# Performance work log

Measured on AMD Instinct MI355X. Metric: run time of the kernel, lower is better.

The kernel has to match this reference:

```python
import jax, jax.numpy as jnp
import numpy as np

B, L, H, X = 64, 512, 1024, 1024
D = H + X  # 2048


def setup_inputs() -> dict:
    key = jax.random.key(0)
    k = jax.random.split(key, 8)
    h_state = jax.random.normal(k[0], (B, L, H), dtype=jnp.float32)
    x = jax.random.normal(k[1], (B, L, X), dtype=jnp.float32)
    trigger = jax.random.randint(k[2], (B, 1), 0, L, dtype=jnp.int64)
    mask = jax.random.randint(k[3], (B, L), 0, 2, dtype=jnp.int32)
    # Linear params (torch Linear: y = x @ W.T + b)
    sa = 1.0 / np.sqrt(D)
    ss = 1.0 / np.sqrt(H)
    W_a = jax.random.uniform(k[4], (D, D), jnp.float32, -sa, sa)
    b_a = jax.random.uniform(k[5], (D,), jnp.float32, -sa, sa)
    W_s = jax.random.uniform(k[6], (D, H), jnp.float32, -ss, ss)
    b_s = jax.random.uniform(k[7], (D,), jnp.float32, -ss, ss)
    return {"h_state": h_state, "x": x, "W_a": W_a, "b_a": b_a,
            "W_s": W_s, "b_s": b_s, "trigger": trigger, "mask": mask}


def reference(h_state, x, W_a, b_a, W_s, b_s, trigger, mask):
    # a: [B, L, D]
    a = jnp.concatenate((h_state, x), axis=-1)
    # direct gather of the trigger position (replaces one_hot+masked_select)
    trig_a = jnp.take_along_axis(a, trigger[:, :, None], axis=1)  # [B, 1, D]
    s = h_state.sum(axis=1)  # [B, H]
    et = jnp.tanh(jnp.einsum('bld,ed->ble', a, W_a) + b_a
                  + (s @ W_s.T + b_s)[:, None, :])  # [B, L, D]
    et = jnp.where(mask[:, :, None] == 0, jnp.float32(-1e9), et)
    attn = jax.nn.softmax(et, axis=-1)  # softmax over feature dim D (as in source)
    # dropout is identity in eval mode
    out = (trig_a * attn).sum(axis=1)  # [B, D]
    return out
```

## Files before the change

kernel.cpp:

```cpp
#include <hip/hip_runtime.h>
#include <cstdint>

#define B_ 64
#define L_ 512
#define H_ 1024
#define D_ 2048

typedef __attribute__((ext_vector_type(8))) short short8;
typedef __attribute__((ext_vector_type(4))) float f32x4;
typedef unsigned int u32;

static __device__ __forceinline__ float bf2f(u32 lo16) {
    u32 u = lo16 << 16;
    return __builtin_bit_cast(float, u);
}
static __device__ __forceinline__ unsigned short f2bf(float f) {
    u32 u = __builtin_bit_cast(u32, f);
    u += 0x7fffu + ((u >> 16) & 1u);
    return (unsigned short)(u >> 16);
}
static __device__ __forceinline__ u32 pk(float x, float y) {
    return (u32)f2bf(x) | ((u32)f2bf(y) << 16);
}
static __device__ __forceinline__ float fast_pexp(float u) {
    u = fminf(15.f, fmaxf(-15.f, u));
    float ex = __expf(2.f * u);
    float th = (ex - 1.f) / (ex + 1.f);
    return __expf(th);
}
static __device__ __forceinline__ void gload_lds16(const unsigned short* g, unsigned short* l) {
    __builtin_amdgcn_global_load_lds((const __attribute__((address_space(1))) u32*)g,
                                     (__attribute__((address_space(3))) u32*)l, 16, 0, 0);
}

__global__ __launch_bounds__(256) void k_s(const float* __restrict__ h, float* __restrict__ s) {
    int t = blockIdx.x * 256 + threadIdx.x;
    int b = t >> 10, hh = t & 1023;
    const float* p = h + ((size_t)b * L_) * H_ + hh;
    float acc = 0.f;
#pragma unroll 8
    for (int l = 0; l < L_; ++l) acc += p[(size_t)l * H_];
    s[t] = acc;
}

__global__ __launch_bounds__(256) void k_compact(const int* __restrict__ mask,
                                                 const float* __restrict__ ba,
                                                 const float* __restrict__ bs,
                                                 int* __restrict__ ridx,
                                                 int* __restrict__ cnt1,
                                                 float* __restrict__ cnt0,
                                                 float* __restrict__ t2) {
    int b = blockIdx.x;
    __shared__ int sm[L_];
    for (int l = threadIdx.x; l < L_; l += 256) sm[l] = mask[b * L_ + l];
    for (int e = threadIdx.x; e < D_; e += 256) t2[b * D_ + e] = ba[e] + bs[e];
    __syncthreads();
    if (threadIdx.x == 0) {
        int* rb = ridx + b * L_;
        int c = 0;
        for (int l = 0; l < L_; ++l) if (sm[l]) rb[c++] = l;
        int n1 = c;
        int last = (c > 0) ? rb[c - 1] : 0;
        for (; c < L_; ++c) rb[c] = last;
        cnt1[b] = n1;
        cnt0[b] = (float)(L_ - n1);
    }
}

__global__ __launch_bounds__(256) void k_cvtW(const float* __restrict__ Wa,
                                              unsigned short* __restrict__ Wb) {
    int t = blockIdx.x * 256 + threadIdx.x;
    float4 v = ((const float4*)Wa)[t];
    ((uint2*)Wb)[t] = make_uint2(pk(v.x, v.y), pk(v.z, v.w));
}

__global__ __launch_bounds__(256) void k_prep(const float* __restrict__ hs, const float* __restrict__ xx,
                                              const int* __restrict__ ridx, const int* __restrict__ cnt1,
                                              unsigned short* __restrict__ Abf) {
    int j = blockIdx.x;
    int b = blockIdx.y;
    int n1 = cnt1[b];
    if (j >= ((n1 + 255) & ~255)) return;
    int l = ridx[b * L_ + j];
    int t = threadIdx.x;
    size_t rb = ((size_t)(b * L_ + l)) << 10;
    const float* src = (t < 128) ? (hs + rb + t * 8) : (xx + rb + (t - 128) * 8);
    float4 v0 = *(const float4*)src;
    float4 v1 = *(const float4*)(src + 4);
    *(uint4*)(Abf + (((size_t)(b * L_ + j)) << 11) + t * 8) =
        make_uint4(pk(v0.x, v0.y), pk(v0.z, v0.w), pk(v1.x, v1.y), pk(v1.z, v1.w));
}

__global__ __launch_bounds__(256) void k_t2(const float* __restrict__ s, const float* __restrict__ Ws,
                                            float* __restrict__ t2) {
    __shared__ float As[16][64];
    __shared__ float Bs[16][64];
    int n0 = blockIdx.x * 64;
    int ks0 = blockIdx.y * 256;
    int tid = threadIdx.x;
    int tx = tid & 15, ty = tid >> 4;
    int r = tid >> 2, q = tid & 3;
    float acc[4][4] = {};
    for (int k0 = ks0; k0 < ks0 + 256; k0 += 16) {
        float4 av = *(const float4*)(s + (size_t)r * H_ + k0 + q * 4);
        float4 bv = *(const float4*)(Ws + (size_t)(n0 + r) * H_ + k0 + q * 4);
        __syncthreads();
        As[q*4+0][r] = av.x; As[q*4+1][r] = av.y; As[q*4+2][r] = av.z; As[q*4+3][r] = av.w;
        Bs[q*4+0][r] = bv.x; Bs[q*4+1][r] = bv.y; Bs[q*4+2][r] = bv.z; Bs[q*4+3][r] = bv.w;
        __syncthreads();
#pragma unroll
        for (int kk = 0; kk < 16; ++kk) {
            float a_[4], b_[4];
            *(float4*)&a_[0] = *(const float4*)&As[kk][ty * 4];
            *(float4*)&b_[0] = *(const float4*)&Bs[kk][tx * 4];
#pragma unroll
            for (int i = 0; i < 4; ++i)
#pragma unroll
                for (int j = 0; j < 4; ++j) acc[i][j] += a_[i] * b_[j];
        }
    }
#pragma unroll
    for (int i = 0; i < 4; ++i)
#pragma unroll
        for (int j = 0; j < 4; ++j)
            atomicAdd(&t2[(size_t)(ty * 4 + i) * D_ + n0 + tx * 4 + j], acc[i][j]);
}

#define BAR3() do { asm volatile("" ::: "memory"); __builtin_amdgcn_s_barrier(); asm volatile("" ::: "memory"); } while (0)

__global__ __launch_bounds__(512, 2) void k_gemm3(
    const unsigned short* __restrict__ Abf, const unsigned short* __restrict__ Wb,
    const float* __restrict__ t2, const int* __restrict__ cnt1,
    float* __restrict__ rowsum, unsigned short* __restrict__ P)
{
    __shared__ unsigned short lds[65536];

    int tid = threadIdx.x;
    int lane = tid & 63;
    int w = tid >> 6;
    int wm = w >> 2;
    int wn = w & 3;
    int g = lane >> 4;
    int cl = lane & 15;

    int n0 = blockIdx.x * 256;
    int jt = blockIdx.y;
    int b = jt >> 1;
    int j0 = (jt & 1) * 256;
    int n1 = cnt1[b];
    if (j0 >= n1) return;

    int sr = w * 16 + (lane & 15);
    int sce = ((lane >> 4) & 3) * 8;
    const unsigned short* aS0 = Abf + (((size_t)(b * L_ + j0 + sr)) << 11) + sce;
    const unsigned short* aS1 = aS0 + ((size_t)128 << 11);
    const unsigned short* bS0 = Wb + (((size_t)(n0 + sr)) << 11) + sce;
    const unsigned short* bS1 = bS0 + ((size_t)128 << 11);
    int wq = w * 512;

#define STAGE_A3(h, tk, u) do { \
        const unsigned short* s_ = ((h) ? aS1 : aS0) + (tk) * 64; \
        unsigned short* d_ = &lds[(u) * 32768 + (h) * 8192 + wq]; \
        gload_lds16(s_, d_); gload_lds16(s_ + 32, d_ + 4096); } while (0)
#define STAGE_B3(h, tk, u) do { \
        const unsigned short* s_ = ((h) ? bS1 : bS0) + (tk) * 64; \
        unsigned short* d_ = &lds[(u) * 32768 + 16384 + (h) * 8192 + wq]; \
        gload_lds16(s_, d_); gload_lds16(s_ + 32, d_ + 4096); } while (0)

    int rdA = wm * 8192 + g * 128 + cl * 8;
    int rdB = 16384 + (wn >> 1) * 8192 + (wn & 1) * 2048 + g * 128 + cl * 8;

    f32x4 acc[8][4] = {};
    short8 af[4][2], bf0[2][2], bf1[2][2];

    STAGE_A3(0, 0, 0); STAGE_B3(0, 0, 0); STAGE_B3(1, 0, 0); STAGE_A3(1, 0, 0);
    STAGE_B3(0, 1, 1); STAGE_B3(1, 1, 1); STAGE_A3(0, 1, 1);
    asm volatile("s_waitcnt vmcnt(6)" ::: "memory");
    BAR3();

    for (int t = 0; t < 32; ++t) {
        int u = t & 1;
        int ub = u * 32768;
        int tn = (t + 1) & 31, tnn = (t + 2) & 31;

#pragma unroll
        for (int m = 0; m < 4; ++m) {
            af[m][0] = *(const short8*)&lds[ub + rdA + m * 512];
            af[m][1] = *(const short8*)&lds[ub + rdA + 4096 + m * 512];
        }
#pragma unroll
        for (int n = 0; n < 2; ++n) {
            bf0[n][0] = *(const short8*)&lds[ub + rdB + n * 512];
            bf0[n][1] = *(const short8*)&lds[ub + rdB + 4096 + n * 512];
        }
        STAGE_A3(1, tn, u ^ 1);
        BAR3();
        __builtin_amdgcn_s_setprio(1);
#pragma unroll
        for (int m = 0; m < 4; ++m)
#pragma unroll
            for (int n = 0; n < 2; ++n) {
                acc[m][n] = __builtin_amdgcn_mfma_f32_16x16x32_bf16(af[m][0], bf0[n][0], acc[m][n], 0, 0, 0);
                acc[m][n] = __builtin_amdgcn_mfma_f32_16x16x32_bf16(af[m][1], bf0[n][1], acc[m][n], 0, 0, 0);
            }
        __builtin_amdgcn_s_setprio(0);
        BAR3();

#pragma unroll
        for (int n = 0; n < 2; ++n) {
            bf1[n][0] = *(const short8*)&lds[ub + rdB + (n + 2) * 512];
            bf1[n][1] = *(const short8*)&lds[ub + rdB + 4096 + (n + 2) * 512];
        }
        BAR3();
        __builtin_amdgcn_s_setprio(1);
#pragma unroll
        for (int m = 0; m < 4; ++m)
#pragma unroll
            for (int n = 0; n < 2; ++n) {
                acc[m][n + 2] = __builtin_amdgcn_mfma_f32_16x16x32_bf16(af[m][0], bf1[n][0], acc[m][n + 2], 0, 0, 0);
                acc[m][n + 2] = __builtin_amdgcn_mfma_f32_16x16x32_bf16(af[m][1], bf1[n][1], acc[m][n + 2], 0, 0, 0);
            }
        __builtin_amdgcn_s_setprio(0);
        BAR3();

#pragma unroll
        for (int m = 0; m < 4; ++m) {
            af[m][0] = *(const short8*)&lds[ub + rdA + (m + 4) * 512];
            af[m][1] = *(const short8*)&lds[ub + rdA + 4096 + (m + 4) * 512];
        }
        STAGE_B3(0, tnn, u);
        BAR3();
        __builtin_amdgcn_s_setprio(1);
#pragma unroll
        for (int m = 0; m < 4; ++m)
#pragma unroll
            for (int n = 0; n < 2; ++n) {
                acc[m + 4][n + 2] = __builtin_amdgcn_mfma_f32_16x16x32_bf16(af[m][0], bf1[n][0], acc[m + 4][n + 2], 0, 0, 0);
                acc[m + 4][n + 2] = __builtin_amdgcn_mfma_f32_16x16x32_bf16(af[m][1], bf1[n][1], acc[m + 4][n + 2], 0, 0, 0);
            }
        __builtin_amdgcn_s_setprio(0);
        BAR3();

        STAGE_B3(1, tnn, u);
        STAGE_A3(0, tnn, u);
        asm volatile("s_waitcnt vmcnt(6)" ::: "memory");
        BAR3();
        __builtin_amdgcn_s_setprio(1);
#pragma unroll
        for (int m = 0; m < 4; ++m)
#pragma unroll
            for (int n = 0; n < 2; ++n) {
                acc[m + 4][n] = __builtin_amdgcn_mfma_f32_16x16x32_bf16(af[m][0], bf0[n][0], acc[m + 4][n], 0, 0, 0);
                acc[m + 4][n] = __builtin_amdgcn_mfma_f32_16x16x32_bf16(af[m][1], bf0[n][1], acc[m + 4][n], 0, 0, 0);
            }
        __builtin_amdgcn_s_setprio(0);
        BAR3();
    }
#undef STAGE_A3
#undef STAGE_B3

    asm volatile("s_waitcnt vmcnt(0)" ::: "memory");
    __syncthreads();

    float t2v[4]; int ecol[4];
#pragma unroll
    for (int n = 0; n < 4; ++n) { ecol[n] = n0 + wn * 64 + n * 16 + cl; t2v[n] = t2[b * D_ + ecol[n]]; }
    int orow0 = b * L_ + j0 + wm * 128;
    int qd = g;

    float rs[8][4] = {};
#pragma unroll
    for (int m = 0; m < 8; ++m) {
        int lrowb = m * 16 + qd * 4;
#pragma unroll
        for (int n = 0; n < 4; ++n) {
#pragma unroll
            for (int gg = 0; gg < 4; ++gg) {
                float p = fast_pexp(acc[m][n][gg] + t2v[n]);
                rs[m][gg] += p;
                P[(size_t)(orow0 + lrowb + gg) * D_ + ecol[n]] = f2bf(p);
            }
        }
    }
#pragma unroll
    for (int m = 0; m < 8; ++m)
#pragma unroll
        for (int gg = 0; gg < 4; ++gg) {
            float v = rs[m][gg];
            v += __shfl_xor(v, 1); v += __shfl_xor(v, 2);
            v += __shfl_xor(v, 4); v += __shfl_xor(v, 8);
            rs[m][gg] = v;
        }
    float* red = (float*)lds;
    if (tid < 256) red[tid] = 0.f;
    __syncthreads();
    if (cl == 0) {
#pragma unroll
        for (int m = 0; m < 8; ++m)
#pragma unroll
            for (int gg = 0; gg < 4; ++gg)
                atomicAdd(&red[wm * 128 + m * 16 + qd * 4 + gg], rs[m][gg]);
    }
    __syncthreads();
    if (tid < 256) atomicAdd(&rowsum[b * L_ + j0 + tid], red[tid]);
}

__global__ __launch_bounds__(256) void k_fin2(const unsigned short* __restrict__ P,
                                              const float* __restrict__ rowsum,
                                              const int* __restrict__ cnt1,
                                              const int* __restrict__ trigger,
                                              const float* __restrict__ hs,
                                              const float* __restrict__ xx,
                                              float* __restrict__ out) {
    int b = blockIdx.y;
    __shared__ float iv[L_];
    int n1 = cnt1[b];
    int lceil = (n1 + 127) & ~127;
    for (int j = threadIdx.x; j < L_; j += 256)
        iv[j] = (j < n1) ? 1.f / rowsum[b * L_ + j] : 0.f;
    __syncthreads();
    int e0 = blockIdx.x * 512 + threadIdx.x * 2;
    const unsigned short* Pb = P + (((size_t)b) << 20) + e0;
    float s0 = 0.f, s1 = 0.f;
#pragma unroll 8
    for (int l = 0; l < lceil; ++l) {
        float f = iv[l];
        u32 pv = *(const u32*)(Pb + (((size_t)l) << 11));
        s0 += f * bf2f(pv & 0xffffu);
        s1 += f * bf2f(pv >> 16);
    }
    float base = (float)(L_ - n1) * (1.f / 2048.f);
    int trig = trigger[b];
    size_t tb = ((size_t)(b * L_ + trig)) << 10;
    float ta0 = (e0 < 1024) ? hs[tb + e0] : xx[tb + e0 - 1024];
    float ta1 = (e0 + 1 < 1024) ? hs[tb + e0 + 1] : xx[tb + e0 + 1 - 1024];
    out[b * D_ + e0]     = (s0 + base) * ta0;
    out[b * D_ + e0 + 1] = (s1 + base) * ta1;
}

#define BM 128
#define BN 128
#define BK 32
#define LDK 40
__global__ __launch_bounds__(256) void k_gemm(
    const float* __restrict__ hs, const float* __restrict__ xx,
    const float* __restrict__ Wa, const unsigned short* __restrict__ Wb,
    const float* __restrict__ t2,
    const int* __restrict__ ridx, const int* __restrict__ cnt1,
    float* __restrict__ rowsum,
    unsigned short* __restrict__ P, float* __restrict__ out, int mode)
{
    __shared__ unsigned short Asl[BM][LDK];
    __shared__ unsigned short Bsl[BN][BK];
    __shared__ float red[BM];

    int tid = threadIdx.x;
    int lane = tid & 63;
    int w = tid >> 6;
    int wm = w & 1, wn = w >> 1;

    int n0 = blockIdx.x * BN;
    int jt = blockIdx.y;
    int b = jt >> 2;
    int j0 = (jt & 3) * BM;
    int n1 = cnt1[b];
    if (j0 >= n1) return;

    int r = tid >> 1;
    int koff = (tid & 1) * 16;
    int l = ridx[b * L_ + j0 + r];
    size_t abase = ((size_t)b * L_ + l) * (size_t)H_;
    const float* hrow = hs + abase;
    const float* xrow = xx + abase;
    const float* browf = Wa + (size_t)(n0 + r) * D_;
    const unsigned short* bw0 = Wb ? Wb + (size_t)(n0 + (tid >> 2)) * D_ + (tid & 3) * 8 : nullptr;
    const unsigned short* bw1 = Wb ? Wb + (size_t)(n0 + 64 + (tid >> 2)) * D_ + (tid & 3) * 8 : nullptr;
    unsigned short* bs0 = &Bsl[0][0] + (size_t)tid * 8;
    unsigned short* bs1 = &Bsl[0][0] + (size_t)(tid + 256) * 8;
    bool useWb = (Wb != nullptr);

    f32x4 acc[4][4] = {};

    for (int k0 = 0; k0 < D_; k0 += BK) {
        int k = k0 + koff;
        const float* ap = (k < H_) ? (hrow + k) : (xrow + (k - H_));
        float4 a0 = *(const float4*)(ap);
        float4 a1 = *(const float4*)(ap + 4);
        float4 a2 = *(const float4*)(ap + 8);
        float4 a3 = *(const float4*)(ap + 12);
        uint4 bv0, bv1;
        float4 c0, c1, c2, c3;
        if (useWb) {
            bv0 = *(const uint4*)(bw0 + k0);
            bv1 = *(const uint4*)(bw1 + k0);
        } else {
            const float* bp = browf + k;
            c0 = *(const float4*)(bp);
            c1 = *(const float4*)(bp + 4);
            c2 = *(const float4*)(bp + 8);
            c3 = *(const float4*)(bp + 12);
        }
        __syncthreads();
        *(uint4*)&Asl[r][koff]     = make_uint4(pk(a0.x,a0.y), pk(a0.z,a0.w), pk(a1.x,a1.y), pk(a1.z,a1.w));
        *(uint4*)&Asl[r][koff + 8] = make_uint4(pk(a2.x,a2.y), pk(a2.z,a2.w), pk(a3.x,a3.y), pk(a3.z,a3.w));
        if (useWb) {
            *(uint4*)bs0 = bv0;
            *(uint4*)bs1 = bv1;
        } else {
            *(uint4*)&Bsl[r][koff]     = make_uint4(pk(c0.x,c0.y), pk(c0.z,c0.w), pk(c1.x,c1.y), pk(c1.z,c1.w));
            *(uint4*)&Bsl[r][koff + 8] = make_uint4(pk(c2.x,c2.y), pk(c2.z,c2.w), pk(c3.x,c3.y), pk(c3.z,c3.w));
        }
        __syncthreads();
        int kb = (lane >> 4) * 8;
        short8 af[4], bfg[4];
#pragma unroll
        for (int i = 0; i < 4; ++i) af[i]  = *(const short8*)&Asl[wm*64 + i*16 + (lane & 15)][kb];
#pragma unroll
        for (int j = 0; j < 4; ++j) bfg[j] = *(const short8*)&Bsl[wn*64 + j*16 + (lane & 15)][kb];
#pragma unroll
        for (int i = 0; i < 4; ++i)
#pragma unroll
            for (int j = 0; j < 4; ++j)
                acc[i][j] = __builtin_amdgcn_mfma_f32_16x16x32_bf16(af[i], bfg[j], acc[i][j], 0, 0, 0);
    }

    int cl = lane & 15, qd = lane >> 4;
    float t2v[4]; int ecol[4];
#pragma unroll
    for (int j = 0; j < 4; ++j) { ecol[j] = n0 + wn*64 + j*16 + cl; t2v[j] = t2[b * D_ + ecol[j]]; }
    int orow0 = b * L_ + j0;

    if (mode <= 1) {
        float rs[4][4] = {};
#pragma unroll
        for (int i = 0; i < 4; ++i) {
            int lrowb = wm*64 + i*16 + qd*4;
#pragma unroll
            for (int j = 0; j < 4; ++j) {
#pragma unroll
                for (int g = 0; g < 4; ++g) {
                    float p = fast_pexp(acc[i][j][g] + t2v[j]);
                    rs[i][g] += p;
                    if (mode == 0)
                        P[(size_t)(orow0 + lrowb + g) * D_ + ecol[j]] = f2bf(p);
                }
            }
        }
#pragma unroll
        for (int i = 0; i < 4; ++i)
#pragma unroll
            for (int g = 0; g < 4; ++g) {
                float v = rs[i][g];
                v += __shfl_xor(v, 1); v += __shfl_xor(v, 2);
                v += __shfl_xor(v, 4); v += __shfl_xor(v, 8);
                rs[i][g] = v;
            }
        __syncthreads();
        if (tid < BM) red[tid] = 0.f;
        __syncthreads();
        if (cl == 0) {
#pragma unroll
            for (int i = 0; i < 4; ++i)
#pragma unroll
                for (int g = 0; g < 4; ++g)
                    atomicAdd(&red[wm*64 + i*16 + qd*4 + g], rs[i][g]);
        }
        __syncthreads();
        if (tid < BM) atomicAdd(&rowsum[orow0 + tid], red[tid]);
    } else {
        float inv[4][4];
#pragma unroll
        for (int i = 0; i < 4; ++i)
#pragma unroll
            for (int g = 0; g < 4; ++g) {
                int lrow = wm*64 + i*16 + qd*4 + g;
                inv[i][g] = (j0 + lrow < n1) ? (1.f / rowsum[orow0 + lrow]) : 0.f;
            }
        float cs[4] = {};
#pragma unroll
        for (int i = 0; i < 4; ++i)
#pragma unroll
            for (int j = 0; j < 4; ++j)
#pragma unroll
                for (int g = 0; g < 4; ++g)
                    cs[j] += fast_pexp(acc[i][j][g] + t2v[j]) * inv[i][g];
#pragma unroll
        for (int j = 0; j < 4; ++j) {
            float v = cs[j];
            v += __shfl_xor(v, 16); v += __shfl_xor(v, 32);
            cs[j] = v;
        }
        __syncthreads();
        if (tid < BN) red[tid] = 0.f;
        __syncthreads();
        if (qd == 0) {
#pragma unroll
            for (int j = 0; j < 4; ++j) atomicAdd(&red[wn*64 + j*16 + cl], cs[j]);
        }
        __syncthreads();
        if (tid < BN) atomicAdd(&out[b * D_ + n0 + tid], red[tid]);
    }
}

__global__ __launch_bounds__(256) void k_inv(const int* __restrict__ cnt1,
                                             const float* __restrict__ rowsum,
                                             float* __restrict__ invr) {
    int t = blockIdx.x * 256 + threadIdx.x;
    int b = t >> 9, j = t & 511;
    invr[t] = (j < cnt1[b]) ? (1.f / rowsum[t]) : 0.f;
}

__global__ __launch_bounds__(256) void k_fin(const unsigned short* __restrict__ P,
                                             const float* __restrict__ invr,
                                             const int* __restrict__ cnt1,
                                             float* __restrict__ out) {
    int b = blockIdx.y;
    int lz = blockIdx.z * 128;
    if (lz >= cnt1[b]) return;
    int e0 = blockIdx.x * 512 + threadIdx.x * 2;
    const unsigned short* Pb = P + ((size_t)b * L_ + lz) * D_ + e0;
    const float* ivb = invr + b * L_ + lz;
    float s0 = 0.f, s1 = 0.f;
    for (int l = 0; l < 128; ++l) {
        float iv = ivb[l];
        u32 pv = *(const u32*)(Pb + (size_t)l * D_);
        s0 += iv * bf2f(pv & 0xffffu);
        s1 += iv * bf2f(pv >> 16);
    }
    atomicAdd(&out[b * D_ + e0], s0);
    atomicAdd(&out[b * D_ + e0 + 1], s1);
}

__global__ __launch_bounds__(256) void k_final(
    const float* __restrict__ hs, const float* __restrict__ xx,
    const int* __restrict__ trigger, const float* __restrict__ cnt0,
    float* __restrict__ out) {
    int t = blockIdx.x * 256 + threadIdx.x;
    int b = t >> 11, e = t & 2047;
    int trig = trigger[b];
    size_t base = ((size_t)b * L_ + trig) * 1024;
    float ta = (e < 1024) ? hs[base + e] : xx[base + e - 1024];
    out[t] = (out[t] + cnt0[b] * (1.0f / 2048.0f)) * ta;
}

extern "C" void kernel_launch(void* const* d_in, const int* in_sizes, int n_in,
                              void* d_out, int out_size, void* d_ws, size_t ws_size,
                              hipStream_t stream) {
    const float* hs = (const float*)d_in[0];
    const float* xx = (const float*)d_in[1];
    const float* Wa = (const float*)d_in[2];
    const float* ba = (const float*)d_in[3];
    const float* Ws = (const float*)d_in[4];
    const float* bs = (const float*)d_in[5];
    const int*   trig = (const int*)d_in[6];
    const int*   mask = (const int*)d_in[7];
    float* out = (float*)d_out;

    float* wsf    = (float*)d_ws;
    float* s      = wsf;
    float* t2     = s + 65536;
    float* cnt0   = t2 + 131072;
    float* rowsum = cnt0 + 64;
    float* invr   = rowsum + 32768;
    int*   cnt1   = (int*)(invr + 32768);
    int*   ridx   = cnt1 + 64;
    unsigned short* P   = (unsigned short*)(ridx + 32768);
    unsigned short* Wb  = P + (size_t)B_ * L_ * D_;
    unsigned short* Abf = Wb + (size_t)D_ * D_;

    const size_t BASE_B   = 1180160ull;
    const size_t NEED_P   = BASE_B + 134217728ull;
    const size_t NEED_WB  = NEED_P + 8388608ull;
    const size_t NEED_ALL = NEED_WB + 134217728ull;
    bool haveP   = ws_size >= NEED_P;
    bool haveWb  = ws_size >= NEED_WB;
    bool haveAll = ws_size >= NEED_ALL;

    (void)hipMemsetAsync(rowsum, 0, (size_t)B_ * L_ * sizeof(float), stream);

    k_s      <<<256, 256, 0, stream>>>(hs, s);
    k_compact<<<B_, 256, 0, stream>>>(mask, ba, bs, ridx, cnt1, cnt0, t2);
    k_t2     <<<dim3(32, 4), 256, 0, stream>>>(s, Ws, t2);

    if (haveAll) {
        k_cvtW <<<4096, 256, 0, stream>>>(Wa, Wb);
        k_prep <<<dim3(512, 64), 256, 0, stream>>>(hs, xx, ridx, cnt1, Abf);
        k_gemm3<<<dim3(8, 128), 512, 0, stream>>>(Abf, Wb, t2, cnt1, rowsum, P);
        k_fin2 <<<dim3(4, 64), 256, 0, stream>>>(P, rowsum, cnt1, trig, hs, xx, out);
    } else {
        dim3 grid(D_ / BN, (B_ * L_) / BM);
        const unsigned short* WbArg = haveWb ? Wb : nullptr;
        if (haveWb) k_cvtW<<<4096, 256, 0, stream>>>(Wa, Wb);
        (void)hipMemsetAsync(out, 0, (size_t)B_ * D_ * sizeof(float), stream);
        if (haveP) {
            k_gemm<<<grid, 256, 0, stream>>>(hs, xx, Wa, WbArg, t2, ridx, cnt1, rowsum, P, out, 0);
            k_inv <<<(B_ * L_) / 256, 256, 0, stream>>>(cnt1, rowsum, invr);
            k_fin <<<dim3(4, 64, 4), 256, 0, stream>>>(P, invr, cnt1, out);
        } else {
            k_gemm<<<grid, 256, 0, stream>>>(hs, xx, Wa, WbArg, t2, ridx, cnt1, rowsum, P, out, 1);
            k_gemm<<<grid, 256, 0, stream>>>(hs, xx, Wa, WbArg, t2, ridx, cnt1, rowsum, P, out, 2);
        }
        k_final<<<(B_ * D_) / 256, 256, 0, stream>>>(hs, xx, trig, cnt0, out);
    }
}
```

Before: 729.4 us.

## Cut main-loop barriers in k_gemm3 and swizzle the grid for tile reuse

The k_gemm3 main loop now runs with two workgroup barriers per K-step instead of eight. All B-fragment reads are issued up front, the MFMA blocks are merged into two larger runs, and the next-stage global-to-LDS copies are issued together mid-iteration. The grid is also transposed and remapped so consecutive blocks work on the same W column tile across different row tiles, aiming for better L2 reuse. With fewer barriers, other waves may still be reading a buffer region when the async LDS stores into it begin, which is a possible race.

Measured after the change: 728.9 us. Within noise of the previous version (-0.1%).

```diff
diff --git a/kernel.cpp b/kernel.cpp
--- a/kernel.cpp
+++ b/kernel.cpp
@@ -143,8 +143,9 @@
     int g = lane >> 4;
     int cl = lane & 15;
 
-    int n0 = blockIdx.x * 256;
-    int jt = blockIdx.y;
+    int bx = blockIdx.x;
+    int jt = ((bx & 7) << 4) | (bx >> 3);
+    int n0 = blockIdx.y * 256;
     int b = jt >> 1;
     int j0 = (jt & 1) * 256;
     int n1 = cnt1[b];
@@ -193,67 +194,59 @@
             bf0[n][0] = *(const short8*)&lds[ub + rdB + n * 512];
             bf0[n][1] = *(const short8*)&lds[ub + rdB + 4096 + n * 512];
         }
-        STAGE_A3(1, tn, u ^ 1);
-        BAR3();
-        __builtin_amdgcn_s_setprio(1);
-#pragma unroll
-        for (int m = 0; m < 4; ++m)
-#pragma unroll
-            for (int n = 0; n < 2; ++n) {
-                acc[m][n] = __builtin_amdgcn_mfma_f32_16x16x32_bf16(af[m][0], bf0[n][0], acc[m][n], 0, 0, 0);
-                acc[m][n] = __builtin_amdgcn_mfma_f32_16x16x32_bf16(af[m][1], bf0[n][1], acc[m][n], 0, 0, 0);
-            }
-        __builtin_amdgcn_s_setprio(0);
-        BAR3();
-
 #pragma unroll
         for (int n = 0; n < 2; ++n) {
             bf1[n][0] = *(const short8*)&lds[ub + rdB + (n + 2) * 512];
             bf1[n][1] = *(const short8*)&lds[ub + rdB + 4096 + (n + 2) * 512];
         }
+        STAGE_A3(1, tn, u ^ 1);
         BAR3();
+
         __builtin_amdgcn_s_setprio(1);
 #pragma unroll
-        for (int m = 0; m < 4; ++m)
-#pragma unroll
-            for (int n = 0; n < 2; ++n) {
-                acc[m][n + 2] = __builtin_amdgcn_mfma_f32_16x16x32_bf16(af[m][0], bf1[n][0], acc[m][n + 2], 0, 0, 0);
-                acc[m][n + 2] = __builtin_amdgcn_mfma_f32_16x16x32_bf16(af[m][1], bf1[n][1], acc[m][n + 2], 0, 0, 0);
-            }
+        for (int h = 0; h < 2; ++h)
+#pragma unroll
+            for (int m = 0; m < 4; ++m)
+#pragma unroll
+                for (int n = 0; n < 2; ++n)
+                    acc[m][n] = __builtin_amdgcn_mfma_f32_16x16x32_bf16(af[m][h], bf0[n][h], acc[m][n], 0, 0, 0);
+#pragma unroll
+        for (int h = 0; h < 2; ++h)
+#pragma unroll
+            for (int m = 0; m < 4; ++m)
+#pragma unroll
+                for (int n = 0; n < 2; ++n)
+                    acc[m][n + 2] = __builtin_amdgcn_mfma_f32_16x16x32_bf16(af[m][h], bf1[n][h], acc[m][n + 2], 0, 0, 0);
         __builtin_amdgcn_s_setprio(0);
-        BAR3();
+
+        STAGE_B3(0, tnn, u);
+        STAGE_B3(1, tnn, u);
+        STAGE_A3(0, tnn, u);
 
 #pragma unroll
         for (int m = 0; m < 4; ++m) {
             af[m][0] = *(const short8*)&lds[ub + rdA + (m + 4) * 512];
             af[m][1] = *(const short8*)&lds[ub + rdA + 4096 + (m + 4) * 512];
         }
-        STAGE_B3(0, tnn, u);
-        BAR3();
+
         __builtin_amdgcn_s_setprio(1);
 #pragma unroll
-        for (int m = 0; m < 4; ++m)
-#pragma unroll
-            for (int n = 0; n < 2; ++n) {
-                acc[m + 4][n + 2] = __builtin_amdgcn_mfma_f32_16x16x32_bf16(af[m][0], bf1[n][0], acc[m + 4][n + 2], 0, 0, 0);
-                acc[m + 4][n + 2] = __builtin_amdgcn_mfma_f32_16x16x32_bf16(af[m][1], bf1[n][1], acc[m + 4][n + 2], 0, 0, 0);
-            }
+        for (int h = 0; h < 2; ++h)
+#pragma unroll
+            for (int m = 0; m < 4; ++m)
+#pragma unroll
+                for (int n = 0; n < 2; ++n)
+                    acc[m + 4][n + 2] = __builtin_amdgcn_mfma_f32_16x16x32_bf16(af[m][h], bf1[n][h], acc[m + 4][n + 2], 0, 0, 0);
+#pragma unroll
+        for (int h = 0; h < 2; ++h)
+#pragma unroll
+            for (int m = 0; m < 4; ++m)
+#pragma unroll
+                for (int n = 0; n < 2; ++n)
+                    acc[m + 4][n] = __builtin_amdgcn_mfma_f32_16x16x32_bf16(af[m][h], bf0[n][h], acc[m + 4][n], 0, 0, 0);
         __builtin_amdgcn_s_setprio(0);
-        BAR3();
-
-        STAGE_B3(1, tnn, u);
-        STAGE_A3(0, tnn, u);
+
         asm volatile("s_waitcnt vmcnt(6)" ::: "memory");
-        BAR3();
-        __builtin_amdgcn_s_setprio(1);
-#pragma unroll
-        for (int m = 0; m < 4; ++m)
-#pragma unroll
-            for (int n = 0; n < 2; ++n) {
-                acc[m + 4][n] = __builtin_amdgcn_mfma_f32_16x16x32_bf16(af[m][0], bf0[n][0], acc[m + 4][n], 0, 0, 0);
-                acc[m + 4][n] = __builtin_amdgcn_mfma_f32_16x16x32_bf16(af[m][1], bf0[n][1], acc[m + 4][n], 0, 0, 0);
-            }
-        __builtin_amdgcn_s_setprio(0);
         BAR3();
     }
 #undef STAGE_A3
@@ -585,7 +578,7 @@
     if (haveAll) {
         k_cvtW <<<4096, 256, 0, stream>>>(Wa, Wb);
         k_prep <<<dim3(512, 64), 256, 0, stream>>>(hs, xx, ridx, cnt1, Abf);
-        k_gemm3<<<dim3(8, 128), 512, 0, stream>>>(Abf, Wb, t2, cnt1, rowsum, P);
+        k_gemm3<<<dim3(128, 8), 512, 0, stream>>>(Abf, Wb, t2, cnt1, rowsum, P);
         k_fin2 <<<dim3(4, 64), 256, 0, stream>>>(P, rowsum, cnt1, trig, hs, xx, out);
     } else {
         dim3 grid(D_ / BN, (B_ * L_) / BM);
```
